# Performance work log

Hardware: AMD Instinct MI355X
Metric: run time of the kernel (lower is better)

The kernel has to match this reference:

```python
import jax, jax.numpy as jnp
import numpy as np

B = 64
FEATS = [96, 64, 64, 64]   # per-level input features
NCNT = [1, 8, 64, 512]     # per-level node counts
NODES = 512                # nodes at current depth (tree[-1])
DEG = 8                    # branching degree at this depth
IN_F = 64                  # features[depth]
OUT_F = 64                 # features[depth+1]
SUP = 640                  # in_f * 10 support hidden


def setup_inputs() -> dict:
    key = jax.random.key(0)
    ks = jax.random.split(key, 12)
    inp = {}
    for i in range(4):
        inp[f"x{i}"] = jax.random.normal(ks[i], (B, NCNT[i], FEATS[i]), jnp.float32)
        inp[f"W{i}"] = jax.random.normal(ks[4 + i], (FEATS[i], OUT_F), jnp.float32) / np.sqrt(FEATS[i]).astype(np.float32)
    inp["branch"] = jax.random.normal(ks[8], (NODES, IN_F, IN_F * DEG), jnp.float32) / np.float32(8.0)
    inp["Ws1"] = jax.random.normal(ks[9], (IN_F, SUP), jnp.float32) / np.float32(8.0)
    inp["Ws2"] = jax.random.normal(ks[10], (SUP, OUT_F), jnp.float32) / np.sqrt(SUP).astype(np.float32)
    bound = np.float32(1.0 / np.sqrt(OUT_F))
    inp["bias"] = jax.random.uniform(ks[11], (1, DEG, OUT_F), jnp.float32, -bound, bound)
    return inp


def _lrelu(v):
    return jnp.where(v > 0, v, 0.2 * v)


def reference(x0, x1, x2, x3, W0, W1, W2, W3, branch, Ws1, Ws2, bias):
    xs = [x0, x1, x2, x3]
    Ws = [W0, W1, W2, W3]
    # multi-depth linear sum: project each ancestor level, replicate each
    # node's vector contiguously down to `NODES` rows (torch repeat+view)
    y = jnp.zeros((B, NODES, OUT_F), jnp.float32)
    for x, W in zip(xs, Ws):
        t = x @ W                                   # (B, n_i, OUT_F)
        y = y + jnp.repeat(t, NODES // t.shape[1], axis=1)
    # branching: per-node weight slice (GEMV per node, shared over batch)
    xb = _lrelu(jnp.einsum('bnf,nfg->bng', x3, branch))  # (B, NODES, IN_F*DEG)
    xb = xb.reshape(B, NODES * DEG, IN_F)
    xb = (xb @ Ws1) @ Ws2                           # support MLP -> (B, NODES*DEG, OUT_F)
    y = xb + jnp.repeat(y, DEG, axis=1)             # y repeat(1,1,deg).view
    y = _lrelu(y + jnp.tile(bias, (1, NODES, 1)))   # bias.repeat(1, nodes, 1)
    return y
```

## Files before the change

kernel.cpp:

```cpp
#include <hip/hip_runtime.h>


typedef float f32x4 __attribute__((ext_vector_type(4)));
typedef __bf16 bf16x8 __attribute__((ext_vector_type(8)));

__device__ __forceinline__ unsigned short f2bf(float f) {
    union { float f; unsigned int u; } x; x.f = f;
    unsigned int r = x.u + 0x7FFFu + ((x.u >> 16) & 1u);
    return (unsigned short)(r >> 16);
}

__global__ __launch_bounds__(256) void tree_prep(
    const float* __restrict__ x0, const float* __restrict__ W0,
    const float* __restrict__ x1, const float* __restrict__ W1,
    const float* __restrict__ x2, const float* __restrict__ W2,
    const float* __restrict__ x3, const float* __restrict__ W3,
    const float* __restrict__ Ws1, const float* __restrict__ Ws2,
    float* __restrict__ ylg, unsigned short* __restrict__ xbf,
    unsigned short* __restrict__ wsF, unsigned short* __restrict__ w3f)
{
    const int t = threadIdx.x;
    const int blk = blockIdx.x;
    if (blk < 512) {
        const int b = blk >> 3, oct = blk & 7;
        const int f = t & 63, gl0 = t >> 6;
        float a0 = 0.f, a1 = 0.f;
        const float* x0p = x0 + b * 96;
        #pragma unroll 8
        for (int k = 0; k < 96; k += 2) {
            a0 += x0p[k]     * W0[k * 64 + f];
            a1 += x0p[k + 1] * W0[(k + 1) * 64 + f];
        }
        const float* x1p = x1 + b * 512 + oct * 64;
        #pragma unroll 8
        for (int k = 0; k < 64; k += 2) {
            a0 += x1p[k]     * W1[k * 64 + f];
            a1 += x1p[k + 1] * W1[(k + 1) * 64 + f];
        }
        const float a01 = a0 + a1;
        const int mt = b >> 4, l4m = (b >> 2) & 3, rm = b & 3;
        const int ft = f >> 4, l15 = f & 15;
        #pragma unroll
        for (int s = 0; s < 2; ++s) {
            const int g = oct * 8 + gl0 + 4 * s;
            const float* x2p = x2 + (size_t)b * 4096 + g * 64;
            float c0 = 0.f, c1 = 0.f;
            #pragma unroll 8
            for (int k = 0; k < 64; k += 2) {
                c0 += x2p[k]     * W2[k * 64 + f];
                c1 += x2p[k + 1] * W2[(k + 1) * 64 + f];
            }
            ylg[(size_t)((g * 4 + mt) * 4 + ft) * 256 + (l4m * 16 + l15) * 4 + rm] =
                a01 + c0 + c1;
        }
    } else if (blk < 1024) {
        const int bb = blk - 512;
        const int b = bb >> 3, q = bb & 7;
        const int n = q * 64 + (t >> 2), kq = t & 3;
        const int mt = b >> 4, l15b = b & 15;
        const float* src = x3 + (size_t)b * 32768 + (size_t)n * 64 + kq * 16;
        #pragma unroll
        for (int i = 0; i < 4; ++i) {
            float4 v = *(const float4*)(src + 4 * i);
            const int k0 = kq * 16 + 4 * i;
            const int ks = k0 >> 5, l4k = (k0 >> 3) & 3, j = k0 & 7;
            union { unsigned short h[4]; uint2 u; } p;
            p.h[0] = f2bf(v.x); p.h[1] = f2bf(v.y); p.h[2] = f2bf(v.z); p.h[3] = f2bf(v.w);
            *(uint2*)&xbf[(size_t)n * 4096 +
                          ((mt * 2 + ks) * 64 + l4k * 16 + l15b) * 8 + j] = p.u;
        }
    } else if (blk < 1088) {
        __shared__ float red[4][64];
        const int c = blk - 1024;
        const int f = t & 63, q = t >> 6;
        const float* w1p = Ws1 + (size_t)c * 640 + q * 160;
        const float* w2p = Ws2 + (size_t)(q * 160) * 64 + f;
        float a0 = 0.f, a1 = 0.f;
        #pragma unroll 8
        for (int s = 0; s < 160; s += 2) {
            a0 += w1p[s]     * w2p[(size_t)s * 64];
            a1 += w1p[s + 1] * w2p[(size_t)(s + 1) * 64];
        }
        red[q][f] = a0 + a1;
        __syncthreads();
        if (q == 0) {
            const float v = red[0][f] + red[1][f] + red[2][f] + red[3][f];
            const int ks = c >> 5, l4c = (c >> 3) & 3, j = c & 7;
            wsF[((f >> 4) * 2 + ks) * 512 + (l4c * 16 + (f & 15)) * 8 + j] = f2bf(v);
        }
    } else {
        const int l = t & 63;
        #pragma unroll
        for (int it = 0; it < 2; ++it) {
            const int fh = it * 4 + (t >> 6);
            const int ft = fh >> 1, ks = fh & 1;
            const int f = ft * 16 + (l & 15);
            const int kb = ks * 32 + (l >> 4) * 8;
            union { unsigned short h[8]; uint4 u; } p;
            #pragma unroll
            for (int j = 0; j < 8; ++j) p.h[j] = f2bf(W3[(kb + j) * 64 + f]);
            *(uint4*)&w3f[((size_t)fh * 64 + l) * 8] = p.u;
        }
    }
}

__global__ __launch_bounds__(256, 3) void tree_main(
    const float* __restrict__ branch, const float* __restrict__ bias,
    const float* __restrict__ ylg, const unsigned short* __restrict__ xbf,
    const unsigned short* __restrict__ wsF, const unsigned short* __restrict__ w3f,
    float* __restrict__ out)
{
    __shared__ unsigned short brB[64 * 258];
    __shared__ unsigned short tsb[4][16 * 72];
    const int t = threadIdx.x;
    const int w = t >> 6, l = t & 63;
    const int l15 = l & 15, l4 = l >> 4;
    const int n = blockIdx.x >> 1, dh = blockIdx.x & 1;
    const int d = 4 * dh + w;
    const int g = n >> 3;
    unsigned short* ts = tsb[w];

    bf16x8 bx[4][2];
    #pragma unroll
    for (int bt = 0; bt < 4; ++bt)
        #pragma unroll
        for (int ks = 0; ks < 2; ++ks)
            bx[bt][ks] = *(const bf16x8*)(xbf + (size_t)n * 4096 +
                                          ((bt * 2 + ks) * 64 + l) * 8);

    {
        const float* bp = branch + (size_t)n * 32768 + dh * 256;
        #pragma unroll
        for (int half = 0; half < 2; ++half) {
            float4 stg[8];
            #pragma unroll
            for (int i = 0; i < 8; ++i) {
                const int fi = (half * 8 + i) * 256 + t;
                const int k = fi >> 6, c4 = (fi & 63) << 2;
                stg[i] = *(const float4*)(bp + (size_t)k * 512 + c4);
            }
            #pragma unroll
            for (int i = 0; i < 8; ++i) {
                const int fi = (half * 8 + i) * 256 + t;
                const int k = fi >> 6, c4 = (fi & 63) << 2;
                union { unsigned short h[4]; uint2 u; } q;
                q.h[0] = f2bf(stg[i].x); q.h[1] = f2bf(stg[i].y);
                q.h[2] = f2bf(stg[i].z); q.h[3] = f2bf(stg[i].w);
                *(uint2*)&brB[k * 258 + c4] = q.u;
            }
        }
    }
    __syncthreads();

    f32x4 yw[4][4];
    #pragma unroll
    for (int bt = 0; bt < 4; ++bt)
        #pragma unroll
        for (int ft = 0; ft < 4; ++ft)
            yw[bt][ft] = *(const f32x4*)(ylg + (size_t)((g * 4 + bt) * 4 + ft) * 256 + l * 4);
    #pragma unroll
    for (int ft = 0; ft < 4; ++ft) {
        bf16x8 w30 = *(const bf16x8*)(w3f + (size_t)((ft * 2 + 0) * 64 + l) * 8);
        bf16x8 w31 = *(const bf16x8*)(w3f + (size_t)((ft * 2 + 1) * 64 + l) * 8);
        #pragma unroll
        for (int bt = 0; bt < 4; ++bt) {
            yw[bt][ft] = __builtin_amdgcn_mfma_f32_16x16x32_bf16(bx[bt][0], w30, yw[bt][ft], 0, 0, 0);
            yw[bt][ft] = __builtin_amdgcn_mfma_f32_16x16x32_bf16(bx[bt][1], w31, yw[bt][ft], 0, 0, 0);
        }
    }

    bf16x8 wf[4][2];
    #pragma unroll
    for (int ft = 0; ft < 4; ++ft)
        #pragma unroll
        for (int ks = 0; ks < 2; ++ks)
            wf[ft][ks] = *(const bf16x8*)(wsF + (size_t)((ft * 2 + ks) * 64 + l) * 8);

    bf16x8 pf[4][2];
    #pragma unroll
    for (int cP = 0; cP < 4; ++cP)
        #pragma unroll
        for (int ks = 0; ks < 2; ++ks) {
            union { unsigned short h[8]; bf16x8 bv; } p;
            #pragma unroll
            for (int j = 0; j < 8; ++j)
                p.h[j] = brB[(32 * ks + 8 * l4 + j) * 258 + w * 64 + 16 * cP + l15];
            pf[cP][ks] = p.bv;
        }

    float* outp = out + (size_t)(n * 8 + d) * 64;
    #pragma unroll
    for (int bt = 0; bt < 4; ++bt) {
        #pragma unroll
        for (int cP = 0; cP < 4; ++cP) {
            f32x4 s = {0.f, 0.f, 0.f, 0.f};
            s = __builtin_amdgcn_mfma_f32_16x16x32_bf16(pf[cP][0], bx[bt][0], s, 0, 0, 0);
            s = __builtin_amdgcn_mfma_f32_16x16x32_bf16(pf[cP][1], bx[bt][1], s, 0, 0, 0);
            union { unsigned short h[4]; uint2 u; } q;
            #pragma unroll
            for (int r = 0; r < 4; ++r) {
                float v = s[r];
                v = fmaxf(v, 0.2f * v);
                q.h[r] = f2bf(v);
            }
            *(uint2*)&ts[l15 * 72 + 16 * cP + 4 * l4] = q.u;
        }
        bf16x8 a20 = *(const bf16x8*)&ts[l15 * 72 + 8 * l4];
        bf16x8 a21 = *(const bf16x8*)&ts[l15 * 72 + 32 + 8 * l4];
        #pragma unroll
        for (int ft = 0; ft < 4; ++ft) {
            f32x4 o = yw[bt][ft];
            o = __builtin_amdgcn_mfma_f32_16x16x32_bf16(a20, wf[ft][0], o, 0, 0, 0);
            o = __builtin_amdgcn_mfma_f32_16x16x32_bf16(a21, wf[ft][1], o, 0, 0, 0);
            const float bv = bias[d * 64 + 16 * ft + l15];
            #pragma unroll
            for (int r = 0; r < 4; ++r) {
                float val = o[r] + bv;
                val = fmaxf(val, 0.2f * val);
                outp[(size_t)(16 * bt + 4 * l4 + r) * 262144 + 16 * ft + l15] = val;
            }
        }
    }
}

extern "C" void kernel_launch(void* const* d_in, const int* in_sizes, int n_in,
                              void* d_out, int out_size, void* d_ws, size_t ws_size,
                              hipStream_t stream) {
    (void)in_sizes; (void)n_in; (void)out_size; (void)ws_size;
    const float* x0     = (const float*)d_in[0];
    const float* W0     = (const float*)d_in[1];
    const float* x1     = (const float*)d_in[2];
    const float* W1     = (const float*)d_in[3];
    const float* x2     = (const float*)d_in[4];
    const float* W2     = (const float*)d_in[5];
    const float* x3     = (const float*)d_in[6];
    const float* W3     = (const float*)d_in[7];
    const float* branch = (const float*)d_in[8];
    const float* Ws1    = (const float*)d_in[9];
    const float* Ws2    = (const float*)d_in[10];
    const float* bias   = (const float*)d_in[11];

    float* ylg          = (float*)d_ws;
    unsigned short* xbf = (unsigned short*)((char*)d_ws + 1048576);
    unsigned short* wsF = (unsigned short*)((char*)d_ws + 5242880);
    unsigned short* w3f = (unsigned short*)((char*)d_ws + 5251072);
    float* out = (float*)d_out;

    tree_prep<<<1089, 256, 0, stream>>>(x0, W0, x1, W1, x2, W2, x3, W3, Ws1, Ws2,
                                        ylg, xbf, wsF, w3f);
    tree_main<<<1024, 256, 0, stream>>>(branch, bias, ylg, xbf, wsF, w3f, out);
}
```

Baseline: 54.48 us.

## Alias scratch LDS over branch tile and stream weights per tile to raise occupancy

The per-wave scratch buffer now reuses the branch-weight LDS region after a barrier, which shrinks the block's LDS footprint. The ylg accumulator array and the hoisted W3/Ws2 fragments are no longer kept in registers up front. They are loaded inside the output loop, where the x3@W3 MFMAs are fused with the support-MLP MFMAs. Launch bounds go from 3 to 4 blocks per CU, trading extra repeated global/L2 loads and one more barrier for lower register and LDS pressure.

```diff
diff --git a/kernel.cpp b/kernel.cpp
--- a/kernel.cpp
+++ b/kernel.cpp
@@ -104,21 +104,19 @@
     }
 }
 
-__global__ __launch_bounds__(256, 3) void tree_main(
+__global__ __launch_bounds__(256, 4) void tree_main(
     const float* __restrict__ branch, const float* __restrict__ bias,
     const float* __restrict__ ylg, const unsigned short* __restrict__ xbf,
     const unsigned short* __restrict__ wsF, const unsigned short* __restrict__ w3f,
     float* __restrict__ out)
 {
-    __shared__ unsigned short brB[64 * 258];
-    __shared__ unsigned short tsb[4][16 * 72];
+    __shared__ unsigned short mem[64 * 258];
     const int t = threadIdx.x;
     const int w = t >> 6, l = t & 63;
     const int l15 = l & 15, l4 = l >> 4;
     const int n = blockIdx.x >> 1, dh = blockIdx.x & 1;
     const int d = 4 * dh + w;
     const int g = n >> 3;
-    unsigned short* ts = tsb[w];
 
     bf16x8 bx[4][2];
     #pragma unroll
@@ -146,35 +144,11 @@
                 union { unsigned short h[4]; uint2 u; } q;
                 q.h[0] = f2bf(stg[i].x); q.h[1] = f2bf(stg[i].y);
                 q.h[2] = f2bf(stg[i].z); q.h[3] = f2bf(stg[i].w);
-                *(uint2*)&brB[k * 258 + c4] = q.u;
+                *(uint2*)&mem[k * 258 + c4] = q.u;
             }
         }
     }
     __syncthreads();
-
-    f32x4 yw[4][4];
-    #pragma unroll
-    for (int bt = 0; bt < 4; ++bt)
-        #pragma unroll
-        for (int ft = 0; ft < 4; ++ft)
-            yw[bt][ft] = *(const f32x4*)(ylg + (size_t)((g * 4 + bt) * 4 + ft) * 256 + l * 4);
-    #pragma unroll
-    for (int ft = 0; ft < 4; ++ft) {
-        bf16x8 w30 = *(const bf16x8*)(w3f + (size_t)((ft * 2 + 0) * 64 + l) * 8);
-        bf16x8 w31 = *(const bf16x8*)(w3f + (size_t)((ft * 2 + 1) * 64 + l) * 8);
-        #pragma unroll
-        for (int bt = 0; bt < 4; ++bt) {
-            yw[bt][ft] = __builtin_amdgcn_mfma_f32_16x16x32_bf16(bx[bt][0], w30, yw[bt][ft], 0, 0, 0);
-            yw[bt][ft] = __builtin_amdgcn_mfma_f32_16x16x32_bf16(bx[bt][1], w31, yw[bt][ft], 0, 0, 0);
-        }
-    }
-
-    bf16x8 wf[4][2];
-    #pragma unroll
-    for (int ft = 0; ft < 4; ++ft)
-        #pragma unroll
-        for (int ks = 0; ks < 2; ++ks)
-            wf[ft][ks] = *(const bf16x8*)(wsF + (size_t)((ft * 2 + ks) * 64 + l) * 8);
 
     bf16x8 pf[4][2];
     #pragma unroll
@@ -184,9 +158,12 @@
             union { unsigned short h[8]; bf16x8 bv; } p;
             #pragma unroll
             for (int j = 0; j < 8; ++j)
-                p.h[j] = brB[(32 * ks + 8 * l4 + j) * 258 + w * 64 + 16 * cP + l15];
+                p.h[j] = mem[(32 * ks + 8 * l4 + j) * 258 + w * 64 + 16 * cP + l15];
             pf[cP][ks] = p.bv;
         }
+    __syncthreads();
+
+    unsigned short* ts = mem + w * (16 * 72);
 
     float* outp = out + (size_t)(n * 8 + d) * 64;
     #pragma unroll
@@ -209,9 +186,15 @@
         bf16x8 a21 = *(const bf16x8*)&ts[l15 * 72 + 32 + 8 * l4];
         #pragma unroll
         for (int ft = 0; ft < 4; ++ft) {
-            f32x4 o = yw[bt][ft];
-            o = __builtin_amdgcn_mfma_f32_16x16x32_bf16(a20, wf[ft][0], o, 0, 0, 0);
-            o = __builtin_amdgcn_mfma_f32_16x16x32_bf16(a21, wf[ft][1], o, 0, 0, 0);
+            f32x4 o = *(const f32x4*)(ylg + (size_t)((g * 4 + bt) * 4 + ft) * 256 + l * 4);
+            bf16x8 w30 = *(const bf16x8*)(w3f + (size_t)((ft * 2 + 0) * 64 + l) * 8);
+            bf16x8 w31 = *(const bf16x8*)(w3f + (size_t)((ft * 2 + 1) * 64 + l) * 8);
+            bf16x8 wf0 = *(const bf16x8*)(wsF + (size_t)((ft * 2 + 0) * 64 + l) * 8);
+            bf16x8 wf1 = *(const bf16x8*)(wsF + (size_t)((ft * 2 + 1) * 64 + l) * 8);
+            o = __builtin_amdgcn_mfma_f32_16x16x32_bf16(bx[bt][0], w30, o, 0, 0, 0);
+            o = __builtin_amdgcn_mfma_f32_16x16x32_bf16(bx[bt][1], w31, o, 0, 0, 0);
+            o = __builtin_amdgcn_mfma_f32_16x16x32_bf16(a20, wf0, o, 0, 0, 0);
+            o = __builtin_amdgcn_mfma_f32_16x16x32_bf16(a21, wf1, o, 0, 0, 0);
             const float bv = bias[d * 64 + 16 * ft + l15];
             #pragma unroll
             for (int r = 0; r < 4; ++r) {
```

New measurement: 47.76 us. 1.14x faster.
